# Optimization experiments

Hardware: AMD Instinct MI355X
Metric: run time of the kernel (lower is better)

Reference implementation:

```python
import jax, jax.numpy as jnp
import numpy as np

N, E, D_IN, H, D_OUT = 50000, 1600000, 256, 128, 64


def setup_inputs() -> dict:
    key = jax.random.key(0)
    ks = jax.random.split(key, 8)
    x = jax.random.normal(ks[0], (N, D_IN), dtype=jnp.float32)
    edge_index = jax.random.randint(ks[1], (2, E), 0, N, dtype=jnp.int64)
    W1 = jax.random.normal(ks[2], (D_IN, H), dtype=jnp.float32) / np.float32(np.sqrt(D_IN))
    b1 = jnp.zeros((H,), jnp.float32)
    W2 = jax.random.normal(ks[3], (H, H), dtype=jnp.float32) / np.float32(np.sqrt(H))
    b2 = jnp.zeros((H,), jnp.float32)
    W3 = jax.random.normal(ks[4], (H, D_OUT), dtype=jnp.float32) / np.float32(np.sqrt(H))
    b3 = jnp.zeros((D_OUT,), jnp.float32)
    return {"x": x, "W1": W1, "b1": b1, "W2": W2, "b2": b2, "W3": W3, "b3": b3,
            "edge_index": edge_index}


def reference(x, W1, b1, W2, b2, W3, b3, edge_index):
    n = x.shape[0]
    # GCN: add self-loops, symmetric normalization D^{-1/2}(A+I)D^{-1/2}
    loop = jnp.arange(n, dtype=edge_index.dtype)
    src = jnp.concatenate([edge_index[0], loop])
    dst = jnp.concatenate([edge_index[1], loop])
    deg = jax.ops.segment_sum(jnp.ones_like(dst, x.dtype), dst, num_segments=n)
    dinv = jnp.where(deg > 0, jax.lax.rsqrt(deg), 0.0).astype(x.dtype)
    norm = dinv[src] * dinv[dst]  # [E+N]

    def gcn_layer(h, W, b):
        h = h @ W                                   # [N, F_out]
        msg = norm[:, None] * h[src]                # gather + scale, [E+N, F_out]
        return jax.ops.segment_sum(msg, dst, num_segments=n) + b

    h = jax.nn.relu(gcn_layer(x, W1, b1))
    h = jax.nn.relu(gcn_layer(h, W2, b2))
    return gcn_layer(h, W3, b3)
```

## Files before the change

kernel.cpp:

```cpp
#include <hip/hip_runtime.h>


constexpr int DIN = 256;
constexpr int HID = 128;
constexpr int DOUT = 64;
constexpr int MAXB = 1024;
constexpr int BSH = 6;
constexpr int EPB = 8192;

typedef unsigned short ushort_t;
typedef unsigned int uint_t;
typedef __attribute__((ext_vector_type(8))) short bf16x8;
typedef __attribute__((ext_vector_type(4))) float f32x4;

__device__ inline ushort_t f2bf(float f) {
  uint_t u = __float_as_uint(f);
  u += 0x7FFF + ((u >> 16) & 1);
  return (ushort_t)(u >> 16);
}
__device__ inline float bf2f(ushort_t b) {
  return __uint_as_float(((uint_t)b) << 16);
}


__device__ inline void wprep_one(const float* __restrict__ W, ushort_t* __restrict__ Bhi,
                                 ushort_t* __restrict__ Blo, int K, int F, int i) {
  int k = i / F, nn = i % F;
  int t = nn >> 4, s = k >> 5, q = (k >> 3) & 3, j = k & 7;
  int lane = q * 16 + (nn & 15);
  int KS = K >> 5;
  size_t idx = (((size_t)t * KS + s) * 64 + (size_t)lane) * 8 + j;
  float w = W[i];
  ushort_t h = f2bf(w);
  float r = w - bf2f(h);
  Bhi[idx] = h;
  Blo[idx] = f2bf(r);
}


__global__ __launch_bounds__(256) void initprep_kernel(
    int* __restrict__ bucket_total, int iblocks,
    const float* __restrict__ W1, ushort_t* __restrict__ W1hi, ushort_t* __restrict__ W1lo,
    const float* __restrict__ W2, ushort_t* __restrict__ W2hi, ushort_t* __restrict__ W2lo,
    const float* __restrict__ W3, ushort_t* __restrict__ W3hi, ushort_t* __restrict__ W3lo) {
  if ((int)blockIdx.x < iblocks) {
    int i = blockIdx.x * 256 + threadIdx.x;
    if (i < MAXB) bucket_total[i] = 0;
  } else {
    int idx = ((int)blockIdx.x - iblocks) * 256 + threadIdx.x;
    constexpr int S1 = DIN * HID;
    constexpr int S2 = S1 + HID * HID;
    constexpr int S3 = S2 + HID * DOUT;
    if (idx < S1) wprep_one(W1, W1hi, W1lo, DIN, HID, idx);
    else if (idx < S2) wprep_one(W2, W2hi, W2lo, HID, HID, idx - S1);
    else if (idx < S3) wprep_one(W3, W3hi, W3lo, HID, DOUT, idx - S2);
  }
}


__global__ __launch_bounds__(256) void bin_kernel(const int* __restrict__ dst, int e,
    int nbuckets, int* __restrict__ bucket_total, int* __restrict__ block_base) {
  __shared__ int h[MAXB];
  int tid = threadIdx.x;
  for (int i = tid; i < nbuckets; i += 256) h[i] = 0;
  __syncthreads();
  int base = blockIdx.x * EPB;
  int end = min(base + EPB, e);
  for (int i = base + tid; i < end; i += 256) atomicAdd(&h[dst[i] >> BSH], 1);
  __syncthreads();
  for (int i = tid; i < nbuckets; i += 256) {
    int v = h[i];
    if (v) block_base[(size_t)blockIdx.x * nbuckets + i] = atomicAdd(&bucket_total[i], v);
  }
}


__global__ __launch_bounds__(256) void scan_buckets_kernel(const int* __restrict__ total,
    int* __restrict__ base, int nb) {
  __shared__ int sums[256];
  int t = threadIdx.x;
  int a[4];
  int ls = 0;
#pragma unroll
  for (int k = 0; k < 4; ++k) {
    int idx = t * 4 + k;
    a[k] = (idx < nb) ? total[idx] : 0;
    ls += a[k];
  }
  sums[t] = ls;
  __syncthreads();
  for (int off = 1; off < 256; off <<= 1) {
    int u = (t >= off) ? sums[t - off] : 0;
    __syncthreads();
    sums[t] += u;
    __syncthreads();
  }
  int run = sums[t] - ls;
#pragma unroll
  for (int k = 0; k < 4; ++k) {
    int idx = t * 4 + k;
    if (idx < nb) base[idx] = run;
    run += a[k];
  }
  if (t == 255) base[nb] = sums[255];
}


template <int K, int F, bool SCALE>
__device__ inline void gemm_mfma_dev(const float* __restrict__ X,
    const ushort_t* __restrict__ Bhi, const ushort_t* __restrict__ Blo,
    const float* __restrict__ dinv, ushort_t* __restrict__ T, int n, int bid) {
  constexpr int NT = F / 16;
  constexpr int KS = K / 32;
  int wave = threadIdx.x >> 6;
  int lane = threadIdx.x & 63;
  int q = lane >> 4;
  int m = lane & 15;
  int arow = bid * 64 + wave * 16 + m;
  bool valid = arow < n;
  const float* xrow = X + (size_t)arow * K;

  f32x4 acc[NT];
#pragma unroll
  for (int t = 0; t < NT; ++t) acc[t] = (f32x4){0.f, 0.f, 0.f, 0.f};

  for (int s = 0; s < KS; ++s) {
    float av[8];
    if (valid) {
      float4 u0 = *(const float4*)(xrow + s * 32 + q * 8);
      float4 u1 = *(const float4*)(xrow + s * 32 + q * 8 + 4);
      av[0] = u0.x; av[1] = u0.y; av[2] = u0.z; av[3] = u0.w;
      av[4] = u1.x; av[5] = u1.y; av[6] = u1.z; av[7] = u1.w;
    } else {
#pragma unroll
      for (int j = 0; j < 8; ++j) av[j] = 0.f;
    }
    bf16x8 ahi, alo;
#pragma unroll
    for (int j = 0; j < 8; ++j) {
      ushort_t h = f2bf(av[j]);
      ahi[j] = (short)h;
      alo[j] = (short)f2bf(av[j] - bf2f(h));
    }
#pragma unroll
    for (int t = 0; t < NT; ++t) {
      size_t boff = (((size_t)t * KS + s) * 64 + (size_t)lane) * 8;
      bf16x8 bh = *(const bf16x8*)(Bhi + boff);
      bf16x8 bl = *(const bf16x8*)(Blo + boff);
      acc[t] = __builtin_amdgcn_mfma_f32_16x16x32_bf16(ahi, bh, acc[t], 0, 0, 0);
      acc[t] = __builtin_amdgcn_mfma_f32_16x16x32_bf16(alo, bh, acc[t], 0, 0, 0);
      acc[t] = __builtin_amdgcn_mfma_f32_16x16x32_bf16(ahi, bl, acc[t], 0, 0, 0);
    }
  }

  int orow_base = bid * 64 + wave * 16 + q * 4;
#pragma unroll
  for (int r = 0; r < 4; ++r) {
    int orow = orow_base + r;
    if (orow >= n) continue;
    float sc = SCALE ? dinv[orow] : 1.0f;
    ushort_t* trow = T + (size_t)orow * F + m;
#pragma unroll
    for (int t = 0; t < NT; ++t) trow[t * 16] = f2bf(sc * acc[t][r]);
  }
}

template <int K, int F>
__global__ __launch_bounds__(256) void gemm_mfma_kernel(const float* __restrict__ X,
    const ushort_t* __restrict__ Bhi, const ushort_t* __restrict__ Blo,
    const float* __restrict__ dinv, ushort_t* __restrict__ T, int n) {
  gemm_mfma_dev<K, F, true>(X, Bhi, Blo, dinv, T, n, blockIdx.x);
}


__global__ __launch_bounds__(256) void fusedA2_kernel(
    const float* __restrict__ X, const ushort_t* __restrict__ Bhi,
    const ushort_t* __restrict__ Blo, ushort_t* __restrict__ T, int n, int gblocks,
    const int* __restrict__ src, const int* __restrict__ dst,
    const int* __restrict__ bucket_base, const int* __restrict__ block_base,
    uint_t* __restrict__ binned, int e, int nbuckets) {
  if ((int)blockIdx.x < gblocks) {
    gemm_mfma_dev<DIN, HID, false>(X, Bhi, Blo, nullptr, T, n, blockIdx.x);
  } else {
    __shared__ int rkh[MAXB];
    __shared__ int cbase[MAXB];
    int tid = threadIdx.x;
    int blk = (int)blockIdx.x - gblocks;
    for (int i = tid; i < nbuckets; i += 256) {
      rkh[i] = 0;
      cbase[i] = bucket_base[i] + block_base[(size_t)blk * nbuckets + i];
    }
    __syncthreads();
    int base = blk * EPB;
    int end = min(base + EPB, e);
    for (int i = base + tid; i < end; i += 256) {
      int d = dst[i];
      int s = src[i];
      int b = d >> BSH;
      int r = atomicAdd(&rkh[b], 1);
      binned[cbase[b] + r] = ((uint_t)d << 16) | (uint_t)s;
    }
  }
}


__global__ __launch_bounds__(256) void csr_kernel(const uint_t* __restrict__ binned,
    const int* __restrict__ bucket_base, int n, int* __restrict__ row_start,
    int* __restrict__ deg, float* __restrict__ dinv, int* __restrict__ col) {
  __shared__ int cnt[64];
  __shared__ int rk[64];
  __shared__ int rs[64];
  __shared__ int ebs[2];
  int tid = threadIdx.x;
  int b = blockIdx.x;
  int node0 = b << BSH;
  if (tid < 64) { cnt[tid] = 0; rk[tid] = 0; }
  if (tid == 0) { ebs[0] = bucket_base[b]; ebs[1] = bucket_base[b + 1]; }
  __syncthreads();
  int ebase = ebs[0];
  int esz = ebs[1] - ebase;
  for (int i = tid; i < esz; i += 256)
    atomicAdd(&cnt[(int)(binned[ebase + i] >> 16) - node0], 1);
  __syncthreads();
  if (tid < 64) {
    int v = cnt[tid];
    int inc = v;
#pragma unroll
    for (int off = 1; off < 64; off <<= 1) {
      int u = __shfl_up(inc, off, 64);
      if (tid >= off) inc += u;
    }
    rs[tid] = inc - v;
    int node = node0 + tid;
    if (node < n) {
      deg[node] = v + 1;
      dinv[node] = rsqrtf((float)(v + 1));
      row_start[node] = ebase + (inc - v);
    }
  }
  __syncthreads();
  for (int i = tid; i < esz; i += 256) {
    uint_t p = binned[ebase + i];
    int l = (int)(p >> 16) - node0;
    int r = atomicAdd(&rk[l], 1);
    col[ebase + rs[l] + r] = (int)(p & 0xFFFFu);
  }
}


template <int F, bool RELU, bool GD>
__global__ __launch_bounds__(256) void spmm_kernel(const ushort_t* __restrict__ t,
    const int* __restrict__ row_start, const int* __restrict__ deg,
    const int* __restrict__ col, const float* __restrict__ dinv,
    const float* __restrict__ bias, float* __restrict__ out, int n) {
  int gw = (int)((blockIdx.x * 256u + threadIdx.x) >> 6);
  int lane = threadIdx.x & 63;
  int n0 = gw * 2;
  int n1 = n0 + 1;
  if (n0 >= n) return;
  bool h1 = (n1 < n);
  int rs0 = row_start[n0], e0 = deg[n0] - 1;
  int rs1 = h1 ? row_start[n1] : 0, e1 = h1 ? (deg[n1] - 1) : 0;
  float di0 = dinv[n0];
  float di1 = h1 ? dinv[n1] : 0.f;

  if constexpr (F == 128) {
    uint_t s0 = ((const uint_t*)(t + (size_t)n0 * F))[lane];
    float ax0 = bf2f((ushort_t)(s0 & 0xFFFF)), ay0 = bf2f((ushort_t)(s0 >> 16));
    if constexpr (GD) { ax0 *= di0; ay0 *= di0; }
    float ax1 = 0.f, ay1 = 0.f;
    if (h1) {
      uint_t s1 = ((const uint_t*)(t + (size_t)n1 * F))[lane];
      ax1 = bf2f((ushort_t)(s1 & 0xFFFF)); ay1 = bf2f((ushort_t)(s1 >> 16));
      if constexpr (GD) { ax1 *= di1; ay1 *= di1; }
    }
    int p0 = rs0, q0 = rs0 + e0;
    int p1 = rs1, q1 = rs1 + e1;
    while (p0 + 4 <= q0 && p1 + 4 <= q1) {
      int c[8];
      uint_t v[8];
      float dc[8];
#pragma unroll
      for (int j = 0; j < 4; ++j) { c[j] = col[p0 + j]; c[4 + j] = col[p1 + j]; }
#pragma unroll
      for (int j = 0; j < 8; ++j) {
        v[j] = ((const uint_t*)(t + (size_t)c[j] * F))[lane];
        if constexpr (GD) dc[j] = dinv[c[j]];
      }
#pragma unroll
      for (int j = 0; j < 4; ++j) {
        if constexpr (GD) {
          ax0 = fmaf(dc[j], bf2f((ushort_t)(v[j] & 0xFFFF)), ax0);
          ay0 = fmaf(dc[j], bf2f((ushort_t)(v[j] >> 16)), ay0);
          ax1 = fmaf(dc[4 + j], bf2f((ushort_t)(v[4 + j] & 0xFFFF)), ax1);
          ay1 = fmaf(dc[4 + j], bf2f((ushort_t)(v[4 + j] >> 16)), ay1);
        } else {
          ax0 += bf2f((ushort_t)(v[j] & 0xFFFF));
          ay0 += bf2f((ushort_t)(v[j] >> 16));
          ax1 += bf2f((ushort_t)(v[4 + j] & 0xFFFF));
          ay1 += bf2f((ushort_t)(v[4 + j] >> 16));
        }
      }
      p0 += 4; p1 += 4;
    }
    for (; p0 + 4 <= q0; p0 += 4) {
      int c[4]; uint_t v[4]; float dc[4];
#pragma unroll
      for (int j = 0; j < 4; ++j) c[j] = col[p0 + j];
#pragma unroll
      for (int j = 0; j < 4; ++j) {
        v[j] = ((const uint_t*)(t + (size_t)c[j] * F))[lane];
        if constexpr (GD) dc[j] = dinv[c[j]];
      }
#pragma unroll
      for (int j = 0; j < 4; ++j) {
        if constexpr (GD) {
          ax0 = fmaf(dc[j], bf2f((ushort_t)(v[j] & 0xFFFF)), ax0);
          ay0 = fmaf(dc[j], bf2f((ushort_t)(v[j] >> 16)), ay0);
        } else {
          ax0 += bf2f((ushort_t)(v[j] & 0xFFFF)); ay0 += bf2f((ushort_t)(v[j] >> 16));
        }
      }
    }
    for (; p0 < q0; ++p0) {
      int c = col[p0];
      uint_t v = ((const uint_t*)(t + (size_t)c * F))[lane];
      float d = GD ? dinv[c] : 1.f;
      if constexpr (GD) {
        ax0 = fmaf(d, bf2f((ushort_t)(v & 0xFFFF)), ax0);
        ay0 = fmaf(d, bf2f((ushort_t)(v >> 16)), ay0);
      } else {
        ax0 += bf2f((ushort_t)(v & 0xFFFF)); ay0 += bf2f((ushort_t)(v >> 16));
      }
    }
    for (; p1 + 4 <= q1; p1 += 4) {
      int c[4]; uint_t v[4]; float dc[4];
#pragma unroll
      for (int j = 0; j < 4; ++j) c[j] = col[p1 + j];
#pragma unroll
      for (int j = 0; j < 4; ++j) {
        v[j] = ((const uint_t*)(t + (size_t)c[j] * F))[lane];
        if constexpr (GD) dc[j] = dinv[c[j]];
      }
#pragma unroll
      for (int j = 0; j < 4; ++j) {
        if constexpr (GD) {
          ax1 = fmaf(dc[j], bf2f((ushort_t)(v[j] & 0xFFFF)), ax1);
          ay1 = fmaf(dc[j], bf2f((ushort_t)(v[j] >> 16)), ay1);
        } else {
          ax1 += bf2f((ushort_t)(v[j] & 0xFFFF)); ay1 += bf2f((ushort_t)(v[j] >> 16));
        }
      }
    }
    for (; p1 < q1; ++p1) {
      int c = col[p1];
      uint_t v = ((const uint_t*)(t + (size_t)c * F))[lane];
      float d = GD ? dinv[c] : 1.f;
      if constexpr (GD) {
        ax1 = fmaf(d, bf2f((ushort_t)(v & 0xFFFF)), ax1);
        ay1 = fmaf(d, bf2f((ushort_t)(v >> 16)), ay1);
      } else {
        ax1 += bf2f((ushort_t)(v & 0xFFFF)); ay1 += bf2f((ushort_t)(v >> 16));
      }
    }
    float bx = bias[2 * lane], by = bias[2 * lane + 1];
    ax0 = fmaf(di0, ax0, bx); ay0 = fmaf(di0, ay0, by);
    if constexpr (RELU) { ax0 = fmaxf(ax0, 0.f); ay0 = fmaxf(ay0, 0.f); }
    float2 o0; o0.x = ax0; o0.y = ay0;
    ((float2*)(out + (size_t)n0 * F))[lane] = o0;
    if (h1) {
      ax1 = fmaf(di1, ax1, bx); ay1 = fmaf(di1, ay1, by);
      if constexpr (RELU) { ax1 = fmaxf(ax1, 0.f); ay1 = fmaxf(ay1, 0.f); }
      float2 o1; o1.x = ax1; o1.y = ay1;
      ((float2*)(out + (size_t)n1 * F))[lane] = o1;
    }
  } else {
    float a0 = bf2f(t[(size_t)n0 * F + lane]);
    float a1 = h1 ? bf2f(t[(size_t)n1 * F + lane]) : 0.f;
    int p0 = rs0, q0 = rs0 + e0;
    int p1 = rs1, q1 = rs1 + e1;
    while (p0 + 4 <= q0 && p1 + 4 <= q1) {
      int c[8];
      ushort_t v[8];
#pragma unroll
      for (int j = 0; j < 4; ++j) { c[j] = col[p0 + j]; c[4 + j] = col[p1 + j]; }
#pragma unroll
      for (int j = 0; j < 8; ++j) v[j] = t[(size_t)c[j] * F + lane];
#pragma unroll
      for (int j = 0; j < 4; ++j) { a0 += bf2f(v[j]); a1 += bf2f(v[4 + j]); }
      p0 += 4; p1 += 4;
    }
    for (; p0 + 4 <= q0; p0 += 4) {
      int c[4]; ushort_t v[4];
#pragma unroll
      for (int j = 0; j < 4; ++j) c[j] = col[p0 + j];
#pragma unroll
      for (int j = 0; j < 4; ++j) v[j] = t[(size_t)c[j] * F + lane];
#pragma unroll
      for (int j = 0; j < 4; ++j) a0 += bf2f(v[j]);
    }
    for (; p0 < q0; ++p0) a0 += bf2f(t[(size_t)col[p0] * F + lane]);
    for (; p1 + 4 <= q1; p1 += 4) {
      int c[4]; ushort_t v[4];
#pragma unroll
      for (int j = 0; j < 4; ++j) c[j] = col[p1 + j];
#pragma unroll
      for (int j = 0; j < 4; ++j) v[j] = t[(size_t)c[j] * F + lane];
#pragma unroll
      for (int j = 0; j < 4; ++j) a1 += bf2f(v[j]);
    }
    for (; p1 < q1; ++p1) a1 += bf2f(t[(size_t)col[p1] * F + lane]);
    float b = bias[lane];
    a0 = fmaf(di0, a0, b);
    if constexpr (RELU) a0 = fmaxf(a0, 0.f);
    out[(size_t)n0 * F + lane] = a0;
    if (h1) {
      a1 = fmaf(di1, a1, b);
      if constexpr (RELU) a1 = fmaxf(a1, 0.f);
      out[(size_t)n1 * F + lane] = a1;
    }
  }
}


extern "C" void kernel_launch(void* const* d_in, const int* in_sizes, int n_in,
                              void* d_out, int out_size, void* d_ws, size_t ws_size,
                              hipStream_t stream) {
  const float* x  = (const float*)d_in[0];
  const float* W1 = (const float*)d_in[1];
  const float* b1 = (const float*)d_in[2];
  const float* W2 = (const float*)d_in[3];
  const float* b2 = (const float*)d_in[4];
  const float* W3 = (const float*)d_in[5];
  const float* b3 = (const float*)d_in[6];
  const int* ei   = (const int*)d_in[7];

  int n = in_sizes[0] / DIN;
  int e = in_sizes[7] / 2;
  const int* src = ei;
  const int* dst = ei + e;

  char* ws = (char*)d_ws;
  size_t off = 0;
  auto alloc = [&](size_t bytes) -> void* {
    off = (off + 255) & ~(size_t)255;
    void* p = ws + off;
    off += bytes;
    return p;
  };
  int nbuckets = (n + 63) >> BSH;
  int nbin = (e + EPB - 1) / EPB;

  int*      bucket_total = (int*)alloc((size_t)MAXB * 4);
  int*      bucket_base  = (int*)alloc((size_t)(MAXB + 1) * 4);
  int*      block_base   = (int*)alloc((size_t)nbin * nbuckets * 4);
  uint_t*   binned       = (uint_t*)alloc((size_t)e * 4);
  int*      deg          = (int*)alloc((size_t)n * 4);
  float*    dinv         = (float*)alloc((size_t)n * 4);
  int*      row_start    = (int*)alloc((size_t)n * 4);
  int*      col          = (int*)alloc((size_t)e * 4);
  ushort_t* T            = (ushort_t*)alloc((size_t)n * HID * 2);
  float*    Hf           = (float*)alloc((size_t)n * HID * 4);
  ushort_t* W1hi         = (ushort_t*)alloc((size_t)DIN * HID * 2);
  ushort_t* W1lo         = (ushort_t*)alloc((size_t)DIN * HID * 2);
  ushort_t* W2hi         = (ushort_t*)alloc((size_t)HID * HID * 2);
  ushort_t* W2lo         = (ushort_t*)alloc((size_t)HID * HID * 2);
  ushort_t* W3hi         = (ushort_t*)alloc((size_t)HID * DOUT * 2);
  ushort_t* W3lo         = (ushort_t*)alloc((size_t)HID * DOUT * 2);
  (void)ws_size;

  int gemm_blocks = (n + 63) / 64;
  int nwaves = (n + 1) / 2;
  int spmm_blocks = (nwaves + 3) / 4;
  constexpr int WPREP_TOTAL = DIN * HID + HID * HID + HID * DOUT;
  int wblocks = (WPREP_TOTAL + 255) / 256;
  int iblocks = MAXB / 256;

  initprep_kernel<<<iblocks + wblocks, 256, 0, stream>>>(
      bucket_total, iblocks,
      W1, W1hi, W1lo, W2, W2hi, W2lo, W3, W3hi, W3lo);
  bin_kernel<<<nbin, 256, 0, stream>>>(dst, e, nbuckets, bucket_total, block_base);
  scan_buckets_kernel<<<1, 256, 0, stream>>>(bucket_total, bucket_base, nbuckets);
  fusedA2_kernel<<<gemm_blocks + nbin, 256, 0, stream>>>(
      x, W1hi, W1lo, T, n, gemm_blocks,
      src, dst, bucket_base, block_base, binned, e, nbuckets);
  csr_kernel<<<nbuckets, 256, 0, stream>>>(binned, bucket_base, n, row_start, deg, dinv, col);

  spmm_kernel<HID, true, true><<<spmm_blocks, 256, 0, stream>>>(T, row_start, deg, col, dinv, b1, Hf, n);
  gemm_mfma_kernel<HID, HID><<<gemm_blocks, 256, 0, stream>>>(Hf, W2hi, W2lo, dinv, T, n);
  spmm_kernel<HID, true, false><<<spmm_blocks, 256, 0, stream>>>(T, row_start, deg, col, dinv, b2, Hf, n);
  gemm_mfma_kernel<HID, DOUT><<<gemm_blocks, 256, 0, stream>>>(Hf, W3hi, W3lo, dinv, T, n);
  spmm_kernel<DOUT, false, false><<<spmm_blocks, 256, 0, stream>>>(T, row_start, deg, col, dinv, b3, (float*)d_out, n);
}
```

Baseline: 354.5 us.

## Fuse SpMM aggregation with the following MFMA GEMM via shared-memory tile

Layer-1 and layer-2 aggregation are merged with the next layer's GEMM. Each block aggregates 32 nodes into an LDS tile, then multiplies that tile by W using split-bf16 MFMA and writes bf16 features scaled by dinv. This removes the fp32 hidden buffer round trip through HBM and two kernel launches. In exchange, each block aggregates only 32 rows with fewer concurrent gathers, and the F=128 spmm_kernel GD path is simplified but no longer launched.

```diff
diff --git a/kernel.cpp b/kernel.cpp
--- a/kernel.cpp
+++ b/kernel.cpp
@@ -163,13 +163,6 @@
 #pragma unroll
     for (int t = 0; t < NT; ++t) trow[t * 16] = f2bf(sc * acc[t][r]);
   }
-}
-
-template <int K, int F>
-__global__ __launch_bounds__(256) void gemm_mfma_kernel(const float* __restrict__ X,
-    const ushort_t* __restrict__ Bhi, const ushort_t* __restrict__ Blo,
-    const float* __restrict__ dinv, ushort_t* __restrict__ T, int n) {
-  gemm_mfma_dev<K, F, true>(X, Bhi, Blo, dinv, T, n, blockIdx.x);
 }
 
 
@@ -248,6 +241,189 @@
 }
 
 
+template <int FOUT, bool GD>
+__global__ __launch_bounds__(256) void spmm_gemm_kernel(
+    const ushort_t* __restrict__ t, const int* __restrict__ row_start,
+    const int* __restrict__ deg, const int* __restrict__ col,
+    const float* __restrict__ dinv, const float* __restrict__ bias,
+    const ushort_t* __restrict__ Bhi, const ushort_t* __restrict__ Blo,
+    ushort_t* __restrict__ Tout, int n) {
+  constexpr int FIN = 128;
+  constexpr int NPB = 32;
+  constexpr int LDW = FIN + 4;
+  __shared__ float agg[NPB][LDW];
+  int wave = threadIdx.x >> 6;
+  int lane = threadIdx.x & 63;
+  int nb0 = (int)blockIdx.x * NPB;
+  float bx = bias[2 * lane], by = bias[2 * lane + 1];
+
+  for (int p = 0; p < 4; ++p) {
+    int ln0 = wave * 8 + 2 * p;
+    int n0 = nb0 + ln0;
+    int n1 = n0 + 1;
+    bool h0 = n0 < n, h1 = n1 < n;
+    int rs0 = h0 ? row_start[n0] : 0, e0 = h0 ? deg[n0] - 1 : 0;
+    int rs1 = h1 ? row_start[n1] : 0, e1 = h1 ? deg[n1] - 1 : 0;
+    float di0 = h0 ? dinv[n0] : 0.f;
+    float di1 = h1 ? dinv[n1] : 0.f;
+    float ax0 = 0.f, ay0 = 0.f, ax1 = 0.f, ay1 = 0.f;
+    if (h0) {
+      uint_t s0 = ((const uint_t*)(t + (size_t)n0 * FIN))[lane];
+      ax0 = bf2f((ushort_t)(s0 & 0xFFFF)); ay0 = bf2f((ushort_t)(s0 >> 16));
+      if constexpr (GD) { ax0 *= di0; ay0 *= di0; }
+    }
+    if (h1) {
+      uint_t s1 = ((const uint_t*)(t + (size_t)n1 * FIN))[lane];
+      ax1 = bf2f((ushort_t)(s1 & 0xFFFF)); ay1 = bf2f((ushort_t)(s1 >> 16));
+      if constexpr (GD) { ax1 *= di1; ay1 *= di1; }
+    }
+    int p0 = rs0, q0 = rs0 + e0;
+    int p1 = rs1, q1 = rs1 + e1;
+    while (p0 + 4 <= q0 && p1 + 4 <= q1) {
+      int c[8];
+      uint_t v[8];
+      float dc[8];
+#pragma unroll
+      for (int j = 0; j < 4; ++j) { c[j] = col[p0 + j]; c[4 + j] = col[p1 + j]; }
+#pragma unroll
+      for (int j = 0; j < 8; ++j) {
+        v[j] = ((const uint_t*)(t + (size_t)c[j] * FIN))[lane];
+        if constexpr (GD) dc[j] = dinv[c[j]];
+      }
+#pragma unroll
+      for (int j = 0; j < 4; ++j) {
+        if constexpr (GD) {
+          ax0 = fmaf(dc[j], bf2f((ushort_t)(v[j] & 0xFFFF)), ax0);
+          ay0 = fmaf(dc[j], bf2f((ushort_t)(v[j] >> 16)), ay0);
+          ax1 = fmaf(dc[4 + j], bf2f((ushort_t)(v[4 + j] & 0xFFFF)), ax1);
+          ay1 = fmaf(dc[4 + j], bf2f((ushort_t)(v[4 + j] >> 16)), ay1);
+        } else {
+          ax0 += bf2f((ushort_t)(v[j] & 0xFFFF));
+          ay0 += bf2f((ushort_t)(v[j] >> 16));
+          ax1 += bf2f((ushort_t)(v[4 + j] & 0xFFFF));
+          ay1 += bf2f((ushort_t)(v[4 + j] >> 16));
+        }
+      }
+      p0 += 4; p1 += 4;
+    }
+    for (; p0 + 4 <= q0; p0 += 4) {
+      int c[4]; uint_t v[4]; float dc[4];
+#pragma unroll
+      for (int j = 0; j < 4; ++j) c[j] = col[p0 + j];
+#pragma unroll
+      for (int j = 0; j < 4; ++j) {
+        v[j] = ((const uint_t*)(t + (size_t)c[j] * FIN))[lane];
+        if constexpr (GD) dc[j] = dinv[c[j]];
+      }
+#pragma unroll
+      for (int j = 0; j < 4; ++j) {
+        if constexpr (GD) {
+          ax0 = fmaf(dc[j], bf2f((ushort_t)(v[j] & 0xFFFF)), ax0);
+          ay0 = fmaf(dc[j], bf2f((ushort_t)(v[j] >> 16)), ay0);
+        } else {
+          ax0 += bf2f((ushort_t)(v[j] & 0xFFFF)); ay0 += bf2f((ushort_t)(v[j] >> 16));
+        }
+      }
+    }
+    for (; p0 < q0; ++p0) {
+      int c = col[p0];
+      uint_t v = ((const uint_t*)(t + (size_t)c * FIN))[lane];
+      if constexpr (GD) {
+        float d = dinv[c];
+        ax0 = fmaf(d, bf2f((ushort_t)(v & 0xFFFF)), ax0);
+        ay0 = fmaf(d, bf2f((ushort_t)(v >> 16)), ay0);
+      } else {
+        ax0 += bf2f((ushort_t)(v & 0xFFFF)); ay0 += bf2f((ushort_t)(v >> 16));
+      }
+    }
+    for (; p1 + 4 <= q1; p1 += 4) {
+      int c[4]; uint_t v[4]; float dc[4];
+#pragma unroll
+      for (int j = 0; j < 4; ++j) c[j] = col[p1 + j];
+#pragma unroll
+      for (int j = 0; j < 4; ++j) {
+        v[j] = ((const uint_t*)(t + (size_t)c[j] * FIN))[lane];
+        if constexpr (GD) dc[j] = dinv[c[j]];
+      }
+#pragma unroll
+      for (int j = 0; j < 4; ++j) {
+        if constexpr (GD) {
+          ax1 = fmaf(dc[j], bf2f((ushort_t)(v[j] & 0xFFFF)), ax1);
+          ay1 = fmaf(dc[j], bf2f((ushort_t)(v[j] >> 16)), ay1);
+        } else {
+          ax1 += bf2f((ushort_t)(v[j] & 0xFFFF)); ay1 += bf2f((ushort_t)(v[j] >> 16));
+        }
+      }
+    }
+    for (; p1 < q1; ++p1) {
+      int c = col[p1];
+      uint_t v = ((const uint_t*)(t + (size_t)c * FIN))[lane];
+      if constexpr (GD) {
+        float d = dinv[c];
+        ax1 = fmaf(d, bf2f((ushort_t)(v & 0xFFFF)), ax1);
+        ay1 = fmaf(d, bf2f((ushort_t)(v >> 16)), ay1);
+      } else {
+        ax1 += bf2f((ushort_t)(v & 0xFFFF)); ay1 += bf2f((ushort_t)(v >> 16));
+      }
+    }
+    float2 o0, o1;
+    o0.x = h0 ? fmaxf(fmaf(di0, ax0, bx), 0.f) : 0.f;
+    o0.y = h0 ? fmaxf(fmaf(di0, ay0, by), 0.f) : 0.f;
+    o1.x = h1 ? fmaxf(fmaf(di1, ax1, bx), 0.f) : 0.f;
+    o1.y = h1 ? fmaxf(fmaf(di1, ay1, by), 0.f) : 0.f;
+    *(float2*)&agg[ln0][2 * lane] = o0;
+    *(float2*)&agg[ln0 + 1][2 * lane] = o1;
+  }
+  __syncthreads();
+
+  constexpr int NT = FOUT / 16;
+  constexpr int KS = FIN / 32;
+  constexpr int NTW = NT / 2;
+  int mt = wave & 1;
+  int g = wave >> 1;
+  int q = lane >> 4, m = lane & 15;
+  f32x4 acc[NTW];
+#pragma unroll
+  for (int tt = 0; tt < NTW; ++tt) acc[tt] = (f32x4){0.f, 0.f, 0.f, 0.f};
+  const float* arow = &agg[mt * 16 + m][0];
+#pragma unroll
+  for (int s = 0; s < KS; ++s) {
+    float4 u0 = *(const float4*)(arow + s * 32 + q * 8);
+    float4 u1 = *(const float4*)(arow + s * 32 + q * 8 + 4);
+    float av[8];
+    av[0] = u0.x; av[1] = u0.y; av[2] = u0.z; av[3] = u0.w;
+    av[4] = u1.x; av[5] = u1.y; av[6] = u1.z; av[7] = u1.w;
+    bf16x8 ahi, alo;
+#pragma unroll
+    for (int j = 0; j < 8; ++j) {
+      ushort_t h = f2bf(av[j]);
+      ahi[j] = (short)h;
+      alo[j] = (short)f2bf(av[j] - bf2f(h));
+    }
+#pragma unroll
+    for (int tt = 0; tt < NTW; ++tt) {
+      int tg = g * NTW + tt;
+      size_t boff = (((size_t)tg * KS + s) * 64 + (size_t)lane) * 8;
+      bf16x8 bh = *(const bf16x8*)(Bhi + boff);
+      bf16x8 bl = *(const bf16x8*)(Blo + boff);
+      acc[tt] = __builtin_amdgcn_mfma_f32_16x16x32_bf16(ahi, bh, acc[tt], 0, 0, 0);
+      acc[tt] = __builtin_amdgcn_mfma_f32_16x16x32_bf16(alo, bh, acc[tt], 0, 0, 0);
+      acc[tt] = __builtin_amdgcn_mfma_f32_16x16x32_bf16(ahi, bl, acc[tt], 0, 0, 0);
+    }
+  }
+  int orow_base = nb0 + mt * 16 + q * 4;
+#pragma unroll
+  for (int r = 0; r < 4; ++r) {
+    int orow = orow_base + r;
+    if (orow >= n) continue;
+    float sc = dinv[orow];
+    ushort_t* trow = Tout + (size_t)orow * FOUT + m;
+#pragma unroll
+    for (int tt = 0; tt < NTW; ++tt) trow[(g * NTW + tt) * 16] = f2bf(sc * acc[tt][r]);
+  }
+}
+
+
 template <int F, bool RELU, bool GD>
 __global__ __launch_bounds__(256) void spmm_kernel(const ushort_t* __restrict__ t,
     const int* __restrict__ row_start, const int* __restrict__ deg,
@@ -267,101 +443,58 @@
   if constexpr (F == 128) {
     uint_t s0 = ((const uint_t*)(t + (size_t)n0 * F))[lane];
     float ax0 = bf2f((ushort_t)(s0 & 0xFFFF)), ay0 = bf2f((ushort_t)(s0 >> 16));
-    if constexpr (GD) { ax0 *= di0; ay0 *= di0; }
     float ax1 = 0.f, ay1 = 0.f;
     if (h1) {
       uint_t s1 = ((const uint_t*)(t + (size_t)n1 * F))[lane];
       ax1 = bf2f((ushort_t)(s1 & 0xFFFF)); ay1 = bf2f((ushort_t)(s1 >> 16));
-      if constexpr (GD) { ax1 *= di1; ay1 *= di1; }
     }
     int p0 = rs0, q0 = rs0 + e0;
     int p1 = rs1, q1 = rs1 + e1;
     while (p0 + 4 <= q0 && p1 + 4 <= q1) {
       int c[8];
       uint_t v[8];
-      float dc[8];
 #pragma unroll
       for (int j = 0; j < 4; ++j) { c[j] = col[p0 + j]; c[4 + j] = col[p1 + j]; }
 #pragma unroll
-      for (int j = 0; j < 8; ++j) {
-        v[j] = ((const uint_t*)(t + (size_t)c[j] * F))[lane];
-        if constexpr (GD) dc[j] = dinv[c[j]];
-      }
-#pragma unroll
-      for (int j = 0; j < 4; ++j) {
-        if constexpr (GD) {
-          ax0 = fmaf(dc[j], bf2f((ushort_t)(v[j] & 0xFFFF)), ax0);
-          ay0 = fmaf(dc[j], bf2f((ushort_t)(v[j] >> 16)), ay0);
-          ax1 = fmaf(dc[4 + j], bf2f((ushort_t)(v[4 + j] & 0xFFFF)), ax1);
-          ay1 = fmaf(dc[4 + j], bf2f((ushort_t)(v[4 + j] >> 16)), ay1);
-        } else {
-          ax0 += bf2f((ushort_t)(v[j] & 0xFFFF));
-          ay0 += bf2f((ushort_t)(v[j] >> 16));
-          ax1 += bf2f((ushort_t)(v[4 + j] & 0xFFFF));
-          ay1 += bf2f((ushort_t)(v[4 + j] >> 16));
-        }
+      for (int j = 0; j < 8; ++j) v[j] = ((const uint_t*)(t + (size_t)c[j] * F))[lane];
+#pragma unroll
+      for (int j = 0; j < 4; ++j) {
+        ax0 += bf2f((ushort_t)(v[j] & 0xFFFF));
+        ay0 += bf2f((ushort_t)(v[j] >> 16));
+        ax1 += bf2f((ushort_t)(v[4 + j] & 0xFFFF));
+        ay1 += bf2f((ushort_t)(v[4 + j] >> 16));
       }
       p0 += 4; p1 += 4;
     }
     for (; p0 + 4 <= q0; p0 += 4) {
-      int c[4]; uint_t v[4]; float dc[4];
+      int c[4]; uint_t v[4];
 #pragma unroll
       for (int j = 0; j < 4; ++j) c[j] = col[p0 + j];
 #pragma unroll
-      for (int j = 0; j < 4; ++j) {
-        v[j] = ((const uint_t*)(t + (size_t)c[j] * F))[lane];
-        if constexpr (GD) dc[j] = dinv[c[j]];
-      }
-#pragma unroll
-      for (int j = 0; j < 4; ++j) {
-        if constexpr (GD) {
-          ax0 = fmaf(dc[j], bf2f((ushort_t)(v[j] & 0xFFFF)), ax0);
-          ay0 = fmaf(dc[j], bf2f((ushort_t)(v[j] >> 16)), ay0);
-        } else {
-          ax0 += bf2f((ushort_t)(v[j] & 0xFFFF)); ay0 += bf2f((ushort_t)(v[j] >> 16));
-        }
+      for (int j = 0; j < 4; ++j) v[j] = ((const uint_t*)(t + (size_t)c[j] * F))[lane];
+#pragma unroll
+      for (int j = 0; j < 4; ++j) {
+        ax0 += bf2f((ushort_t)(v[j] & 0xFFFF)); ay0 += bf2f((ushort_t)(v[j] >> 16));
       }
     }
     for (; p0 < q0; ++p0) {
-      int c = col[p0];
-      uint_t v = ((const uint_t*)(t + (size_t)c * F))[lane];
-      float d = GD ? dinv[c] : 1.f;
-      if constexpr (GD) {
-        ax0 = fmaf(d, bf2f((ushort_t)(v & 0xFFFF)), ax0);
-        ay0 = fmaf(d, bf2f((ushort_t)(v >> 16)), ay0);
-      } else {
-        ax0 += bf2f((ushort_t)(v & 0xFFFF)); ay0 += bf2f((ushort_t)(v >> 16));
-      }
+      uint_t v = ((const uint_t*)(t + (size_t)col[p0] * F))[lane];
+      ax0 += bf2f((ushort_t)(v & 0xFFFF)); ay0 += bf2f((ushort_t)(v >> 16));
     }
     for (; p1 + 4 <= q1; p1 += 4) {
-      int c[4]; uint_t v[4]; float dc[4];
+      int c[4]; uint_t v[4];
 #pragma unroll
       for (int j = 0; j < 4; ++j) c[j] = col[p1 + j];
 #pragma unroll
-      for (int j = 0; j < 4; ++j) {
-        v[j] = ((const uint_t*)(t + (size_t)c[j] * F))[lane];
-        if constexpr (GD) dc[j] = dinv[c[j]];
-      }
-#pragma unroll
-      for (int j = 0; j < 4; ++j) {
-        if constexpr (GD) {
-          ax1 = fmaf(dc[j], bf2f((ushort_t)(v[j] & 0xFFFF)), ax1);
-          ay1 = fmaf(dc[j], bf2f((ushort_t)(v[j] >> 16)), ay1);
-        } else {
-          ax1 += bf2f((ushort_t)(v[j] & 0xFFFF)); ay1 += bf2f((ushort_t)(v[j] >> 16));
-        }
+      for (int j = 0; j < 4; ++j) v[j] = ((const uint_t*)(t + (size_t)c[j] * F))[lane];
+#pragma unroll
+      for (int j = 0; j < 4; ++j) {
+        ax1 += bf2f((ushort_t)(v[j] & 0xFFFF)); ay1 += bf2f((ushort_t)(v[j] >> 16));
       }
     }
     for (; p1 < q1; ++p1) {
-      int c = col[p1];
-      uint_t v = ((const uint_t*)(t + (size_t)c * F))[lane];
-      float d = GD ? dinv[c] : 1.f;
-      if constexpr (GD) {
-        ax1 = fmaf(d, bf2f((ushort_t)(v & 0xFFFF)), ax1);
-        ay1 = fmaf(d, bf2f((ushort_t)(v >> 16)), ay1);
-      } else {
-        ax1 += bf2f((ushort_t)(v & 0xFFFF)); ay1 += bf2f((ushort_t)(v >> 16));
-      }
+      uint_t v = ((const uint_t*)(t + (size_t)col[p1] * F))[lane];
+      ax1 += bf2f((ushort_t)(v & 0xFFFF)); ay1 += bf2f((ushort_t)(v >> 16));
     }
     float bx = bias[2 * lane], by = bias[2 * lane + 1];
     ax0 = fmaf(di0, ax0, bx); ay0 = fmaf(di0, ay0, by);
@@ -459,8 +592,8 @@
   float*    dinv         = (float*)alloc((size_t)n * 4);
   int*      row_start    = (int*)alloc((size_t)n * 4);
   int*      col          = (int*)alloc((size_t)e * 4);
-  ushort_t* T            = (ushort_t*)alloc((size_t)n * HID * 2);
-  float*    Hf           = (float*)alloc((size_t)n * HID * 4);
+  ushort_t* Ta           = (ushort_t*)alloc((size_t)n * HID * 2);
+  ushort_t* Tb           = (ushort_t*)alloc((size_t)n * HID * 2);
   ushort_t* W1hi         = (ushort_t*)alloc((size_t)DIN * HID * 2);
   ushort_t* W1lo         = (ushort_t*)alloc((size_t)DIN * HID * 2);
   ushort_t* W2hi         = (ushort_t*)alloc((size_t)HID * HID * 2);
@@ -470,6 +603,7 @@
   (void)ws_size;
 
   int gemm_blocks = (n + 63) / 64;
+  int sg_blocks = (n + 31) / 32;
   int nwaves = (n + 1) / 2;
   int spmm_blocks = (nwaves + 3) / 4;
   constexpr int WPREP_TOTAL = DIN * HID + HID * HID + HID * DOUT;
@@ -482,13 +616,14 @@
   bin_kernel<<<nbin, 256, 0, stream>>>(dst, e, nbuckets, bucket_total, block_base);
   scan_buckets_kernel<<<1, 256, 0, stream>>>(bucket_total, bucket_base, nbuckets);
   fusedA2_kernel<<<gemm_blocks + nbin, 256, 0, stream>>>(
-      x, W1hi, W1lo, T, n, gemm_blocks,
+      x, W1hi, W1lo, Ta, n, gemm_blocks,
       src, dst, bucket_base, block_base, binned, e, nbuckets);
   csr_kernel<<<nbuckets, 256, 0, stream>>>(binned, bucket_base, n, row_start, deg, dinv, col);
 
-  spmm_kernel<HID, true, true><<<spmm_blocks, 256, 0, stream>>>(T, row_start, deg, col, dinv, b1, Hf, n);
-  gemm_mfma_kernel<HID, HID><<<gemm_blocks, 256, 0, stream>>>(Hf, W2hi, W2lo, dinv, T, n);
-  spmm_kernel<HID, true, false><<<spmm_blocks, 256, 0, stream>>>(T, row_start, deg, col, dinv, b2, Hf, n);
-  gemm_mfma_kernel<HID, DOUT><<<gemm_blocks, 256, 0, stream>>>(Hf, W3hi, W3lo, dinv, T, n);
-  spmm_kernel<DOUT, false, false><<<spmm_blocks, 256, 0, stream>>>(T, row_start, deg, col, dinv, b3, (float*)d_out, n);
-}
+  spmm_gemm_kernel<HID, true><<<sg_blocks, 256, 0, stream>>>(
+      Ta, row_start, deg, col, dinv, b1, W2hi, W2lo, Tb, n);
+  spmm_gemm_kernel<DOUT, false><<<sg_blocks, 256, 0, stream>>>(
+      Tb, row_start, deg, col, dinv, b2, W3hi, W3lo, Ta, n);
+  spmm_kernel<DOUT, false, false><<<spmm_blocks, 256, 0, stream>>>(
+      Ta, row_start, deg, col, dinv, b3, (float*)d_out, n);
+}
```

New measurement: 358.6 us. About the same (+1.2%).
